# Kernel tuning notes

Hardware: AMD Instinct MI355X
Metric: run time of the kernel (lower is better)

Reference implementation:

```python
import jax, jax.numpy as jnp
import numpy as np

# Static block node counts (src of layer l has N[l] nodes, dst has N[l+1])
N = [100000, 50000, 25000, 12500]
E = [750000, 250000, 125000]
D = 128          # in_feats == n_hidden
E_PAIR = 10000   # pos/neg pair-graph edges
BN_EPS = 1e-5


def setup_inputs() -> dict:
    key = jax.random.key(0)
    ks = jax.random.split(key, 32)
    inp = {}
    inp['x'] = jax.random.normal(ks[0], (N[0], D), dtype=jnp.float32)
    for l in range(3):
        inp[f'src{l}'] = jax.random.randint(ks[1 + 2 * l], (E[l],), 0, N[l], dtype=jnp.int32)
        inp[f'dst{l}'] = jax.random.randint(ks[2 + 2 * l], (E[l],), 0, N[l + 1], dtype=jnp.int32)
    inp['perm'] = jax.random.permutation(ks[7], N[0]).astype(jnp.int32)
    inp['pos_src'] = jax.random.randint(ks[8], (E_PAIR,), 0, N[3], dtype=jnp.int32)
    inp['pos_dst'] = jax.random.randint(ks[9], (E_PAIR,), 0, N[3], dtype=jnp.int32)
    inp['neg_src'] = jax.random.randint(ks[10], (E_PAIR,), 0, N[3], dtype=jnp.int32)
    inp['neg_dst'] = jax.random.randint(ks[11], (E_PAIR,), 0, N[3], dtype=jnp.int32)
    s = 1.0 / np.sqrt(D)
    ki = 12
    for l in range(3):
        inp[f'Wself{l}'] = jax.random.normal(ks[ki], (D, D), dtype=jnp.float32) * s; ki += 1
        inp[f'Wneigh{l}'] = jax.random.normal(ks[ki], (D, D), dtype=jnp.float32) * s; ki += 1
        inp[f'b{l}'] = jnp.zeros((D,), dtype=jnp.float32)
    for l in range(2):
        inp[f'gamma{l}'] = jnp.ones((D,), dtype=jnp.float32)
        inp[f'beta{l}'] = jnp.zeros((D,), dtype=jnp.float32)
    inp['disc_W'] = jax.random.uniform(ks[ki], (D, D), dtype=jnp.float32, minval=-s, maxval=s); ki += 1
    inp['pW1'] = jax.random.normal(ks[ki], (D, D), dtype=jnp.float32) * s; ki += 1
    inp['pb1'] = jnp.zeros((D,), dtype=jnp.float32)
    inp['pW2'] = jax.random.normal(ks[ki], (D, D), dtype=jnp.float32) * s; ki += 1
    inp['pb2'] = jnp.zeros((D,), dtype=jnp.float32)
    inp['pW3'] = jax.random.normal(ks[ki], (D, 1), dtype=jnp.float32) * s; ki += 1
    inp['pb3'] = jnp.zeros((1,), dtype=jnp.float32)
    return inp


def _sage(h, src, dst, n_dst, Wself, Wneigh, b):
    # DGL SAGEConv('mean'): fc_self(h_dst) + fc_neigh(mean over in-neighbors)
    agg = jax.ops.segment_sum(h[src], dst, num_segments=n_dst)          # [n_dst, D]
    deg = jax.ops.segment_sum(jnp.ones(src.shape, h.dtype), dst, num_segments=n_dst)
    mean = agg / jnp.clip(deg, 1.0)[:, None]
    return h[:n_dst] @ Wself + mean @ Wneigh + b


def _bn(h, g, b):
    m = h.mean(0)
    v = h.var(0)
    return g * (h - m) * jax.lax.rsqrt(v + BN_EPS) + b


def _encode(h, blocks, params):
    for l in range(3):
        src, dst, n_dst = blocks[l]
        Ws, Wn, b, g, be = params[l]
        h = _sage(h, src, dst, n_dst, Ws, Wn, b)
        if l != 2:
            h = jax.nn.relu(_bn(h, g, be))  # dropout rate 0
    return h


def reference(x, src0, dst0, src1, dst1, src2, dst2, perm,
              pos_src, pos_dst, neg_src, neg_dst,
              Wself0, Wneigh0, b0, Wself1, Wneigh1, b1, Wself2, Wneigh2, b2,
              gamma0, beta0, gamma1, beta1, disc_W,
              pW1, pb1, pW2, pb2, pW3, pb3):
    blocks = [(src0, dst0, N[1]), (src1, dst1, N[2]), (src2, dst2, N[3])]
    params = [(Wself0, Wneigh0, b0, gamma0, beta0),
              (Wself1, Wneigh1, b1, gamma1, beta1),
              (Wself2, Wneigh2, b2, None, None)]
    positive = _encode(x, blocks, params)          # [N3, D]
    negative = _encode(x[perm], blocks, params)    # corruption: permuted features
    summary = jax.nn.sigmoid(positive.mean(0))     # [D]
    ws = disc_W @ summary                          # [D]
    pos = positive @ ws                            # [N3]
    neg = negative @ ws
    l1 = jnp.mean(jax.nn.softplus(-pos))           # BCEWithLogits vs ones
    l2 = jnp.mean(jax.nn.softplus(neg))            # BCEWithLogits vs zeros

    def predictor(z):
        z = jax.nn.relu(z @ pW1 + pb1)
        z = jax.nn.relu(z @ pW2 + pb2)
        return z @ pW3 + pb3

    h_pos = predictor(positive[pos_src] * positive[pos_dst])  # [E_PAIR, 1]
    h_neg = predictor(positive[neg_src] * positive[neg_dst])
    return h_pos, h_neg, l1 + l2
```

## Files before the change

kernel.cpp:

```cpp
#include <hip/hip_runtime.h>
#include <hip/hip_bf16.h>

#define DD 128
#define BN_EPS 1e-5f
#define NBLK 160
#define ALD 264
#define PLD 136

typedef __hip_bfloat16 bf16;
typedef __attribute__((ext_vector_type(8))) short short8;
typedef __attribute__((ext_vector_type(4))) float f32x4;

__device__ __forceinline__ float b2f(unsigned short u) {
    union { float f; unsigned int i; } x; x.i = ((unsigned int)u) << 16; return x.f;
}
__device__ __forceinline__ unsigned short f2bs(float v) {
    bf16 h = __float2bfloat16(v);
    return *(unsigned short*)&h;
}

__global__ void detect_dtype(const unsigned int* __restrict__ x, int* __restrict__ flag) {
    __shared__ int s[256];
    int t = threadIdx.x;
    unsigned int u = x[t];
    unsigned int e = (u >> 7) & 0xFFu;
    s[t] = ((e >= 90u && e <= 140u) || ((u & 0xFFFFu) == 0u)) ? 1 : 0;
    __syncthreads();
    for (int off = 128; off > 0; off >>= 1) { if (t < off) s[t] += s[t + off]; __syncthreads(); }
    if (t == 0) *flag = (s[0] >= 128) ? 1 : 0;
}

struct CvtTable {
    const void* src[20];
    int off[20];
    int n[20];
    int total;
};
__global__ __launch_bounds__(256) void cvt_all(CvtTable tab, float* __restrict__ wsf,
                                               const int* __restrict__ flagp) {
    int i = blockIdx.x * 256 + threadIdx.x;
    if (i >= tab.total) return;
    int k = 0;
    while (i >= tab.n[k]) { i -= tab.n[k]; ++k; }
    float v;
    if (*flagp) v = b2f(((const unsigned short*)tab.src[k])[i]);
    else        v = ((const float*)tab.src[k])[i];
    wsf[tab.off[k] + i] = v;
}

struct WfAll {
    const float* W1[5];
    const float* W2[5];
    unsigned short* dst[5];
    int KS[5];
    int start[5];
    int total;
};
__global__ __launch_bounds__(256) void wfrag_all(WfAll w) {
    int t = blockIdx.x * 256 + threadIdx.x;
    if (t >= w.total) return;
    int k = 0;
    while (k < 4 && t >= w.start[k + 1]) ++k;
    int lt = t - w.start[k];
    int KS = w.KS[k];
    int lane = lt & 63;
    int ks = (lt >> 6) % KS;
    int ct = lt / (KS * 64);
    int n = ct * 16 + (lane & 15);
    unsigned short v[8];
#pragma unroll
    for (int j = 0; j < 8; ++j) {
        int kk = ks * 32 + ((lane >> 4) & 3) * 8 + j;
        float wv = (kk < 128) ? w.W1[k][kk * DD + n] : w.W2[k][(kk - 128) * DD + n];
        v[j] = f2bs(wv);
    }
    *(uint4*)&w.dst[k][(size_t)lt * 8] = *(uint4*)v;
}

__global__ __launch_bounds__(256) void hist_win(
    const int* __restrict__ d0, int e0, const int* __restrict__ d1, int e1,
    const int* __restrict__ d2, int e2, int* __restrict__ hist) {
    int stride = gridDim.x * 256;
    int t0 = blockIdx.x * 256 + threadIdx.x;
    for (int w = 0; w < 4; ++w) {
        int dlo = w * 12500, dhi = dlo + 12500;
        for (int e = t0; e < e0; e += stride) {
            int d = d0[e];
            if (d >= dlo && d < dhi) atomicAdd(&hist[d], 1);
        }
    }
    for (int e = t0; e < e1; e += stride) atomicAdd(&hist[50000 + d1[e]], 1);
    for (int e = t0; e < e2; e += stride) atomicAdd(&hist[75000 + d2[e]], 1);
}

__global__ __launch_bounds__(256) void scan_bsum(const int* __restrict__ cnt, int n,
                                                 int* __restrict__ bsums) {
    __shared__ int sm[256];
    int t = threadIdx.x, b = blockIdx.x;
    int i4 = b * 256 + t;
    int local = 0;
    if (i4 * 4 < n) { int4 v = ((const int4*)cnt)[i4]; local = v.x + v.y + v.z + v.w; }
    sm[t] = local;
    __syncthreads();
    for (int off = 128; off > 0; off >>= 1) { if (t < off) sm[t] += sm[t + off]; __syncthreads(); }
    if (t == 0) bsums[b] = sm[0];
}
__global__ void scan_bscan(int* __restrict__ bsums, int nb, int* __restrict__ rowptr_n) {
    __shared__ int wsum[4];
    int t = threadIdx.x, lane = t & 63, w = t >> 6;
    int v = (t < nb) ? bsums[t] : 0;
    int inc = v;
    for (int off = 1; off < 64; off <<= 1) {
        int u = __shfl_up(inc, off, 64);
        if (lane >= off) inc += u;
    }
    if (lane == 63) wsum[w] = inc;
    __syncthreads();
    int wo = 0;
    for (int i = 0; i < w; ++i) wo += wsum[i];
    if (t < nb) bsums[t] = wo + inc - v;
    if (t == 255) *rowptr_n = wo + inc;
}
__global__ __launch_bounds__(256) void scan_apply(const int* __restrict__ cnt, int n,
                                                  const int* __restrict__ bsums,
                                                  int* __restrict__ rowptr) {
    __shared__ int wsum[4];
    int t = threadIdx.x, b = blockIdx.x, lane = t & 63, w = t >> 6;
    int i4 = b * 256 + t;
    int4 v = {0, 0, 0, 0};
    bool valid = (i4 * 4 < n);
    if (valid) v = ((const int4*)cnt)[i4];
    int local = v.x + v.y + v.z + v.w;
    int inc = local;
    for (int off = 1; off < 64; off <<= 1) {
        int u = __shfl_up(inc, off, 64);
        if (lane >= off) inc += u;
    }
    if (lane == 63) wsum[w] = inc;
    __syncthreads();
    int wo = 0;
    for (int i = 0; i < w; ++i) wo += wsum[i];
    if (valid) {
        int acc = bsums[b] + wo + inc - local;
        int base = i4 * 4;
        rowptr[base + 0] = acc; acc += v.x;
        rowptr[base + 1] = acc; acc += v.y;
        rowptr[base + 2] = acc; acc += v.z;
        rowptr[base + 3] = acc;
    }
}

__global__ __launch_bounds__(256) void csr_fill_win(
    const int* __restrict__ s0, const int* __restrict__ d0, int e0,
    const int* __restrict__ s1, const int* __restrict__ d1, int e1,
    const int* __restrict__ s2, const int* __restrict__ d2, int e2,
    const int* __restrict__ rpAll, int* __restrict__ cur, int* __restrict__ eid) {
    int stride = gridDim.x * 256;
    int t0 = blockIdx.x * 256 + threadIdx.x;
    for (int w = 0; w < 4; ++w) {
        int dlo = w * 12500, dhi = dlo + 12500;
        for (int e = t0; e < e0; e += stride) {
            int d = d0[e];
            if (d >= dlo && d < dhi)
                eid[rpAll[d] + atomicAdd(&cur[d], 1)] = s0[e];
        }
    }
    for (int e = t0; e < e1; e += stride) {
        int gd = 50000 + d1[e];
        eid[rpAll[gd] + atomicAdd(&cur[gd], 1)] = s1[e];
    }
    for (int e = t0; e < e2; e += stride) {
        int gd = 75000 + d2[e];
        eid[rpAll[gd] + atomicAdd(&cur[gd], 1)] = s2[e];
    }
}

__global__ __launch_bounds__(256) void gather2(
    const void* __restrict__ hvP, const void* __restrict__ hvN,
    const int* __restrict__ flagp,
    const int* __restrict__ permP, const int* __restrict__ permN,
    const float* __restrict__ scP, const float* __restrict__ shP,
    const float* __restrict__ scN, const float* __restrict__ shN,
    const int* __restrict__ rowptr, const int* __restrict__ eid,
    int N, int nRows, unsigned short* __restrict__ out)
{
    int row = blockIdx.x * 4 + (threadIdx.x >> 6);
    int lane = threadIdx.x & 63;
    if (row >= nRows) return;
    int half = row >= N;
    int d = half ? row - N : row;
    const void* hv = half ? hvN : hvP;
    const int* perm = half ? permN : permP;
    const float* sc = half ? scN : scP;
    const float* sh = half ? shN : shP;
    int i0 = rowptr[d], i1 = rowptr[d + 1];
    int abf = flagp ? *flagp : 1;
    bool bn = (sc != nullptr);
    float c0 = 1.0f, c1 = 1.0f, h0 = 0.0f, h1 = 0.0f;
    if (bn) { c0 = sc[lane * 2]; c1 = sc[lane * 2 + 1]; h0 = sh[lane * 2]; h1 = sh[lane * 2 + 1]; }

#define XF0(v) (bn ? fmaxf(c0 * (v) + h0, 0.0f) : (v))
#define XF1(v) (bn ? fmaxf(c1 * (v) + h1, 0.0f) : (v))
    float ax[8] = {}, ay[8] = {};
    int i = i0;
    if (abf) {
        const unsigned short* h = (const unsigned short*)hv;
        for (; i + 8 <= i1; i += 8) {
            int sI[8];
#pragma unroll
            for (int j = 0; j < 8; ++j) sI[j] = eid[i + j];
            if (perm) {
#pragma unroll
                for (int j = 0; j < 8; ++j) sI[j] = perm[sI[j]];
            }
            ushort2 v[8];
#pragma unroll
            for (int j = 0; j < 8; ++j) v[j] = *(const ushort2*)&h[(size_t)sI[j] * DD + lane * 2];
#pragma unroll
            for (int j = 0; j < 8; ++j) { ax[j] += XF0(b2f(v[j].x)); ay[j] += XF1(b2f(v[j].y)); }
        }
        for (; i < i1; ++i) {
            int s = eid[i];
            if (perm) s = perm[s];
            ushort2 v = *(const ushort2*)&h[(size_t)s * DD + lane * 2];
            ax[0] += XF0(b2f(v.x)); ay[0] += XF1(b2f(v.y));
        }
    } else {
        const float* h = (const float*)hv;
        for (; i + 8 <= i1; i += 8) {
            int sI[8];
#pragma unroll
            for (int j = 0; j < 8; ++j) sI[j] = eid[i + j];
            if (perm) {
#pragma unroll
                for (int j = 0; j < 8; ++j) sI[j] = perm[sI[j]];
            }
            float2 v[8];
#pragma unroll
            for (int j = 0; j < 8; ++j) v[j] = *(const float2*)&h[(size_t)sI[j] * DD + lane * 2];
#pragma unroll
            for (int j = 0; j < 8; ++j) { ax[j] += XF0(v[j].x); ay[j] += XF1(v[j].y); }
        }
        for (; i < i1; ++i) {
            int s = eid[i];
            if (perm) s = perm[s];
            float2 v = *(const float2*)&h[(size_t)s * DD + lane * 2];
            ax[0] += XF0(v.x); ay[0] += XF1(v.y);
        }
    }
#undef XF0
#undef XF1
    float sx = (ax[0] + ax[1]) + (ax[2] + ax[3]) + (ax[4] + ax[5]) + (ax[6] + ax[7]);
    float sy = (ay[0] + ay[1]) + (ay[2] + ay[3]) + (ay[4] + ay[5]) + (ay[6] + ay[7]);
    float rd = 1.0f / fmaxf((float)(i1 - i0), 1.0f);
    ushort2 o;
    o.x = f2bs(sx * rd);
    o.y = f2bs(sy * rd);
    *(ushort2*)&out[(size_t)row * DD + lane * 2] = o;
}

struct GHalf {
    const void* A1;
    const int* gather;
    const float* sc;
    const float* sh;
    const unsigned short* A2;
    unsigned short* out;
    float* PS;
    float* PQ;
};
__global__ __launch_bounds__(256) void mfma_gemm2(
    GHalf hP, GHalf hN, const int* __restrict__ flagp,
    const uint4* __restrict__ wfrag, const float* __restrict__ bias,
    int Nh, int nbHalf)
{
    __shared__ unsigned short As[64 * ALD];
    __shared__ float sds[256];
    const int tid = threadIdx.x;
    const int half = blockIdx.x / nbHalf;
    const int rb = (blockIdx.x % nbHalf) * 64;
    const GHalf H = half ? hN : hP;
    const int abf = flagp ? *flagp : 1;
    const bool bn = (H.sc != nullptr);
    const bool doStats = (H.PS != nullptr);

    {
        int r = tid >> 2, cs = (tid & 3) * 32;
        int gr = rb + r;
        unsigned short* dst = &As[r * ALD + cs];
        if (gr < Nh) {
            int ar = H.gather ? H.gather[gr] : gr;
            if (abf) {
                const unsigned short* s = (const unsigned short*)H.A1 + (size_t)ar * DD + cs;
                if (bn) {
#pragma unroll
                    for (int i = 0; i < 32; ++i) {
                        float v = b2f(s[i]);
                        v = fmaxf(H.sc[cs + i] * v + H.sh[cs + i], 0.0f);
                        dst[i] = f2bs(v);
                    }
                } else {
                    const uint4* sv = (const uint4*)s;
                    uint4* dv = (uint4*)dst;
#pragma unroll
                    for (int i = 0; i < 4; ++i) dv[i] = sv[i];
                }
            } else {
                const float* s = (const float*)H.A1 + (size_t)ar * DD + cs;
#pragma unroll
                for (int i = 0; i < 32; ++i) dst[i] = f2bs(s[i]);
            }
            const uint4* s2 = (const uint4*)(H.A2 + (size_t)gr * DD + cs);
            uint4* d2 = (uint4*)(dst + 128);
#pragma unroll
            for (int i = 0; i < 4; ++i) d2[i] = s2[i];
        } else {
            uint4 z = {0, 0, 0, 0};
            uint4* dv = (uint4*)dst;
#pragma unroll
            for (int i = 0; i < 4; ++i) dv[i] = z;
            uint4* d2 = (uint4*)(dst + 128);
#pragma unroll
            for (int i = 0; i < 4; ++i) d2[i] = z;
        }
    }
    if (doStats) { sds[tid] = 0.0f; }
    __syncthreads();

    const int w = tid >> 6, lane = tid & 63;
    const int m0 = w * 16;
    f32x4 acc[8] = {};
    for (int ks = 0; ks < 8; ++ks) {
        short8 a = *(const short8*)&As[(m0 + (lane & 15)) * ALD + ks * 32 + ((lane >> 4) & 3) * 8];
#pragma unroll
        for (int ct = 0; ct < 8; ++ct) {
            uint4 braw = wfrag[(ct * 8 + ks) * 64 + lane];
            short8 b = *(short8*)&braw;
            acc[ct] = __builtin_amdgcn_mfma_f32_16x16x32_bf16(a, b, acc[ct], 0, 0, 0);
        }
    }

#pragma unroll
    for (int ct = 0; ct < 8; ++ct) {
        int col = ct * 16 + (lane & 15);
        float bv = bias[col];
        float sv = 0.0f, sq = 0.0f;
#pragma unroll
        for (int r = 0; r < 4; ++r) {
            int grow = rb + m0 + ((lane >> 4) & 3) * 4 + r;
            float v = acc[ct][r] + bv;
            if (grow < Nh) {
                H.out[(size_t)grow * DD + col] = f2bs(v);
                sv += v; sq += v * v;
            }
        }
        if (doStats) {
            sv += __shfl_down(sv, 32, 64); sv += __shfl_down(sv, 16, 64);
            sq += __shfl_down(sq, 32, 64); sq += __shfl_down(sq, 16, 64);
            if (lane < 16) {
                atomicAdd(&sds[ct * 16 + lane], sv);
                atomicAdd(&sds[128 + ct * 16 + lane], sq);
            }
        }
    }
    if (doStats) {
        __syncthreads();
        if (tid < 128) {
            H.PS[(blockIdx.x % nbHalf) * 128 + tid] = sds[tid];
            H.PQ[(blockIdx.x % nbHalf) * 128 + tid] = sds[128 + tid];
        }
    }
}

__global__ __launch_bounds__(256) void pred_gemm(
    const unsigned short* __restrict__ A,
    const unsigned short* __restrict__ PF,
    const int* __restrict__ ps, const int* __restrict__ pd,
    const int* __restrict__ ns, const int* __restrict__ nd, int EPc,
    const uint4* __restrict__ wfrag, const float* __restrict__ bias,
    unsigned short* __restrict__ out, int Mc)
{
    __shared__ unsigned short As[64 * PLD];
    const int tid = threadIdx.x;
    const int rb = blockIdx.x * 64;

    {
        int r = tid >> 2, cs = (tid & 3) * 32;
        int gr = rb + r;
        unsigned short* dst = &As[r * PLD + cs];
        if (gr < Mc) {
            if (ps) {
                int a = (gr < EPc) ? ps[gr] : ns[gr - EPc];
                int b = (gr < EPc) ? pd[gr] : nd[gr - EPc];
                const unsigned short* ra = PF + (size_t)a * DD + cs;
                const unsigned short* rbp = PF + (size_t)b * DD + cs;
#pragma unroll
                for (int i = 0; i < 32; ++i)
                    dst[i] = f2bs(b2f(ra[i]) * b2f(rbp[i]));
            } else {
                const uint4* sv = (const uint4*)(A + (size_t)gr * DD + cs);
                uint4* dv = (uint4*)dst;
#pragma unroll
                for (int i = 0; i < 4; ++i) dv[i] = sv[i];
            }
        } else {
            uint4 z = {0, 0, 0, 0};
            uint4* dv = (uint4*)dst;
#pragma unroll
            for (int i = 0; i < 4; ++i) dv[i] = z;
        }
    }
    __syncthreads();

    const int w = tid >> 6, lane = tid & 63;
    const int m0 = w * 16;
    f32x4 acc[8] = {};
    for (int ks = 0; ks < 4; ++ks) {
        short8 a = *(const short8*)&As[(m0 + (lane & 15)) * PLD + ks * 32 + ((lane >> 4) & 3) * 8];
#pragma unroll
        for (int ct = 0; ct < 8; ++ct) {
            uint4 braw = wfrag[(ct * 4 + ks) * 64 + lane];
            short8 b = *(short8*)&braw;
            acc[ct] = __builtin_amdgcn_mfma_f32_16x16x32_bf16(a, b, acc[ct], 0, 0, 0);
        }
    }

#pragma unroll
    for (int ct = 0; ct < 8; ++ct) {
        int col = ct * 16 + (lane & 15);
        float bv = bias[col];
#pragma unroll
        for (int r = 0; r < 4; ++r) {
            int grow = rb + m0 + ((lane >> 4) & 3) * 4 + r;
            if (grow >= Mc) continue;
            float v = fmaxf(acc[ct][r] + bv, 0.0f);
            out[(size_t)grow * DD + col] = f2bs(v);
        }
    }
}

__global__ __launch_bounds__(256) void p2bn_fast(
    const float* __restrict__ PSa, const float* __restrict__ PQa,
    float* __restrict__ sca, float* __restrict__ sha,
    const float* __restrict__ PSb, const float* __restrict__ PQb,
    float* __restrict__ scb, float* __restrict__ shb,
    int nb, int M,
    const float* __restrict__ gamma, const float* __restrict__ beta)
{
    int tensor = blockIdx.x >> 7, col = blockIdx.x & 127;
    const float* PS = tensor ? PSb : PSa;
    const float* PQ = tensor ? PQb : PQa;
    float* sc = tensor ? scb : sca;
    float* sh = tensor ? shb : sha;
    __shared__ float sS[256], sQ[256];
    int t = threadIdx.x;
    float s = 0.0f, q = 0.0f;
    for (int b = t; b < nb; b += 256) {
        s += PS[b * 128 + col];
        q += PQ[b * 128 + col];
    }
    sS[t] = s; sQ[t] = q;
    __syncthreads();
    for (int off = 128; off > 0; off >>= 1) {
        if (t < off) { sS[t] += sS[t + off]; sQ[t] += sQ[t + off]; }
        __syncthreads();
    }
    if (t == 0) {
        float m = sS[0] / (float)M;
        float var = fmaxf(sQ[0] / (float)M - m * m, 0.0f);
        float inv = rsqrtf(var + BN_EPS);
        float g = gamma[col];
        sc[col] = g * inv;
        sh[col] = beta[col] - g * m * inv;
    }
}

__global__ __launch_bounds__(256) void colreduce(const float* __restrict__ PS, int nb,
                                                 float* __restrict__ out) {
    __shared__ float sS[256];
    int col = blockIdx.x;
    int t = threadIdx.x;
    float s = 0.0f;
    for (int b = t; b < nb; b += 256) s += PS[b * 128 + col];
    sS[t] = s;
    __syncthreads();
    for (int off = 128; off > 0; off >>= 1) { if (t < off) sS[t] += sS[t + off]; __syncthreads(); }
    if (t == 0) out[col] = sS[0];
}

__global__ void make_ws(const float* __restrict__ colsum, const float* __restrict__ discW,
                        float* __restrict__ wsv, int M) {
    __shared__ float s[128];
    int t = threadIdx.x;
    s[t] = 1.0f / (1.0f + expf(-(colsum[t] / (float)M)));
    __syncthreads();
    float acc = 0.0f;
#pragma unroll
    for (int j = 0; j < 128; ++j) acc += discW[t * 128 + j] * s[j];
    wsv[t] = acc;
}

__global__ __launch_bounds__(256) void loss_partial(
    const unsigned short* __restrict__ P, const unsigned short* __restrict__ Ng,
    const float* __restrict__ wsv, float* __restrict__ lossP, float* __restrict__ lossN, int M)
{
    __shared__ float sP[4], sN[4];
    int lane = threadIdx.x & 63;
    int wave = threadIdx.x >> 6;
    int gw = blockIdx.x * 4 + wave;
    int nw = gridDim.x * 4;
    float w0 = wsv[lane], w1 = wsv[lane + 64];
    float accP = 0.0f, accN = 0.0f;
    for (int row = gw; row < 2 * M; row += nw) {
        const unsigned short* base = (row < M) ? &P[(size_t)row * DD]
                                               : &Ng[(size_t)(row - M) * DD];
        float a = b2f(base[lane]) * w0 + b2f(base[lane + 64]) * w1;
#pragma unroll
        for (int off = 32; off > 0; off >>= 1) a += __shfl_down(a, off, 64);
        if (lane == 0) {
            float x = (row < M) ? -a : a;
            float sp = fmaxf(x, 0.0f) + log1pf(expf(-fabsf(x)));
            if (row < M) accP += sp; else accN += sp;
        }
    }
    if (lane == 0) { sP[wave] = accP; sN[wave] = accN; }
    __syncthreads();
    if (threadIdx.x == 0) {
        lossP[blockIdx.x] = sP[0] + sP[1] + sP[2] + sP[3];
        lossN[blockIdx.x] = sN[0] + sN[1] + sN[2] + sN[3];
    }
}

__global__ void write_loss(const float* __restrict__ lossP, const float* __restrict__ lossN,
                           void* __restrict__ outv, int M, const int* __restrict__ flagp) {
    __shared__ float s[256];
    int t = threadIdx.x;
    s[t] = (t < NBLK) ? (lossP[t] + lossN[t]) : 0.0f;
    __syncthreads();
    for (int off = 128; off > 0; off >>= 1) { if (t < off) s[t] += s[t + off]; __syncthreads(); }
    if (t == 0) {
        float v = s[0] / (float)M;
        if (*flagp) ((bf16*)outv)[20000] = __float2bfloat16(v);
        else        ((float*)outv)[20000] = v;
    }
}

__global__ __launch_bounds__(256) void final_mv(
    const unsigned short* __restrict__ ZB, const float* __restrict__ pW3,
    const float* __restrict__ pb3,
    void* __restrict__ outv, int nRows, const int* __restrict__ flagp) {
    int row = blockIdx.x * 4 + (threadIdx.x >> 6);
    int lane = threadIdx.x & 63;
    if (row >= nRows) return;
    float a = b2f(ZB[(size_t)row * DD + lane]) * pW3[lane]
            + b2f(ZB[(size_t)row * DD + lane + 64]) * pW3[lane + 64];
#pragma unroll
    for (int off = 32; off > 0; off >>= 1) a += __shfl_down(a, off, 64);
    if (lane == 0) {
        float v = a + pb3[0];
        if (*flagp) ((bf16*)outv)[row] = __float2bfloat16(v);
        else        ((float*)outv)[row] = v;
    }
}

extern "C" void kernel_launch(void* const* d_in, const int* in_sizes, int n_in,
                              void* d_out, int out_size, void* d_ws, size_t ws_size,
                              hipStream_t stream)
{
    const void* x      = d_in[0];
    const int* srcA[3] = {(const int*)d_in[1], (const int*)d_in[3], (const int*)d_in[5]};
    const int* dstA[3] = {(const int*)d_in[2], (const int*)d_in[4], (const int*)d_in[6]};
    const int* perm    = (const int*)d_in[7];
    const int* pos_src = (const int*)d_in[8];
    const int* pos_dst = (const int*)d_in[9];
    const int* neg_src = (const int*)d_in[10];
    const int* neg_dst = (const int*)d_in[11];

    const int N1 = 50000, N2 = 25000, N3 = 12500;
    const int E[3] = {750000, 250000, 125000};
    const int EP = 10000;
    const int NCAT = 87500;

    float* wsf = (float*)d_ws;
    int*   wsi = (int*)d_ws;
    int*   flagp = wsi;
    float* lossP = wsf + 64;
    float* lossN = wsf + 224;
    float* wsvec = wsf + 512;
    float* scP0 = wsf + 640;  float* shP0 = wsf + 768;
    float* scN0 = wsf + 896;  float* shN0 = wsf + 1024;
    float* scP1 = wsf + 1152; float* shP1 = wsf + 1280;
    float* scN1 = wsf + 1408; float* shN1 = wsf + 1536;
    int*   bsums = wsi + 1664;
    float* colsum = wsf + 1920;
    float* PSP = wsf + 2048;
    float* PQP = wsf + 102400;
    float* PSN = wsf + 202752;
    float* PQN = wsf + 303104;
    int* histAll = wsi + 403456;
    int* curAll  = wsi + 491008;
    int* rpAll   = wsi + 578560;
    int* eidAll  = wsi + 666112;
    const size_t WfB = 1791232;
    float* WS[3] = {wsf + WfB, wsf + WfB + 32896, wsf + WfB + 65792};
    float* WN[3] = {wsf + WfB + 16384, wsf + WfB + 49280, wsf + WfB + 82176};
    float* BV[3] = {wsf + WfB + 32768, wsf + WfB + 65664, wsf + WfB + 98560};
    float* G0  = wsf + WfB + 98688;  float* BE0 = wsf + WfB + 98816;
    float* G1  = wsf + WfB + 98944;  float* BE1 = wsf + WfB + 99072;
    float* DW  = wsf + WfB + 99200;
    float* PW1 = wsf + WfB + 115584; float* PB1 = wsf + WfB + 131968;
    float* PW2 = wsf + WfB + 132096; float* PB2 = wsf + WfB + 148480;
    float* PW3 = wsf + WfB + 148608; float* PB3 = wsf + WfB + 148736;
    unsigned short* wfragL[3] = {(unsigned short*)(wsf + 1940480),
                                 (unsigned short*)(wsf + 1956864),
                                 (unsigned short*)(wsf + 1973248)};
    unsigned short* wfragP[2] = {(unsigned short*)(wsf + 1989632),
                                 (unsigned short*)(wsf + 1997824)};
    unsigned short* PF  = (unsigned short*)(wsf + 2006016);
    unsigned short* NF  = (unsigned short*)(wsf + 2806016);
    unsigned short* H2P = (unsigned short*)(wsf + 3606016);
    unsigned short* H2N = (unsigned short*)(wsf + 5206016);
    unsigned short* H1P = (unsigned short*)(wsf + 6806016);
    unsigned short* H1N = (unsigned short*)(wsf + 10006016);
    unsigned short* AGG = (unsigned short*)(wsf + 13206016);
    unsigned short* ZA = H1N;
    unsigned short* ZB = H1N + (size_t)2560000;

    detect_dtype<<<1, 256, 0, stream>>>((const unsigned int*)x, flagp);
    CvtTable tab;
    const int widx[20] = {12,13,14, 15,16,17, 18,19,20, 21,22,23,24, 25, 26,27, 28,29, 30,31};
    float* wdst[20] = {WS[0],WN[0],BV[0], WS[1],WN[1],BV[1], WS[2],WN[2],BV[2],
                       G0,BE0,G1,BE1, DW, PW1,PB1, PW2,PB2, PW3,PB3};
    const int wn[20] = {16384,16384,128, 16384,16384,128, 16384,16384,128,
                        128,128,128,128, 16384, 16384,128, 16384,128, 128,1};
    int tot = 0;
    for (int k = 0; k < 20; ++k) {
        tab.src[k] = d_in[widx[k]];
        tab.off[k] = (int)(wdst[k] - wsf);
        tab.n[k] = wn[k];
        tot += wn[k];
    }
    tab.total = tot;
    cvt_all<<<(tot + 255) / 256, 256, 0, stream>>>(tab, wsf, flagp);

    hipMemsetAsync(histAll, 0, (size_t)(2 * NCAT + 128) * 4, stream);
    hist_win<<<512, 256, 0, stream>>>(dstA[0], E[0], dstA[1], E[1], dstA[2], E[2], histAll);
    {
        int nb = (NCAT / 4 + 255) / 256;
        scan_bsum<<<nb, 256, 0, stream>>>(histAll, NCAT, bsums);
        scan_bscan<<<1, 256, 0, stream>>>(bsums, nb, rpAll + NCAT);
        scan_apply<<<nb, 256, 0, stream>>>(histAll, NCAT, bsums, rpAll);
    }
    csr_fill_win<<<512, 256, 0, stream>>>(
        srcA[0], dstA[0], E[0], srcA[1], dstA[1], E[1], srcA[2], dstA[2], E[2],
        rpAll, curAll, eidAll);

    WfAll wa;
    wa.W1[0] = WS[0]; wa.W2[0] = WN[0]; wa.dst[0] = wfragL[0]; wa.KS[0] = 8; wa.start[0] = 0;
    wa.W1[1] = WS[1]; wa.W2[1] = WN[1]; wa.dst[1] = wfragL[1]; wa.KS[1] = 8; wa.start[1] = 4096;
    wa.W1[2] = WS[2]; wa.W2[2] = WN[2]; wa.dst[2] = wfragL[2]; wa.KS[2] = 8; wa.start[2] = 8192;
    wa.W1[3] = PW1;   wa.W2[3] = nullptr; wa.dst[3] = wfragP[0]; wa.KS[3] = 4; wa.start[3] = 12288;
    wa.W1[4] = PW2;   wa.W2[4] = nullptr; wa.dst[4] = wfragP[1]; wa.KS[4] = 4; wa.start[4] = 14336;
    wa.total = 16384;
    wfrag_all<<<64, 256, 0, stream>>>(wa);

    const int nb0 = (N1 + 63) / 64, nb1 = (N2 + 63) / 64, nb2 = (N3 + 63) / 64;

    gather2<<<(N1 + 3) / 4, 256, 0, stream>>>(
        x, x, flagp, nullptr, nullptr, nullptr, nullptr, nullptr, nullptr,
        rpAll, eidAll, N1, N1, AGG);
    {
        GHalf hP = {x, nullptr, nullptr, nullptr, AGG, H1P, PSP, PQP};
        mfma_gemm2<<<nb0, 256, 0, stream>>>(hP, hP, flagp, (const uint4*)wfragL[0], BV[0], N1, nb0);
    }
    gather2<<<(N1 + 3) / 4, 256, 0, stream>>>(
        x, x, flagp, perm, perm, nullptr, nullptr, nullptr, nullptr,
        rpAll, eidAll, N1, N1, AGG);
    {
        GHalf hN = {x, perm, nullptr, nullptr, AGG, H1N, PSN, PQN};
        mfma_gemm2<<<nb0, 256, 0, stream>>>(hN, hN, flagp, (const uint4*)wfragL[0], BV[0], N1, nb0);
    }
    p2bn_fast<<<256, 256, 0, stream>>>(PSP, PQP, scP0, shP0, PSN, PQN, scN0, shN0, nb0, N1, G0, BE0);

    gather2<<<(2 * N2 + 3) / 4, 256, 0, stream>>>(
        H1P, H1N, nullptr, nullptr, nullptr, scP0, shP0, scN0, shN0,
        rpAll + 50000, eidAll, N2, 2 * N2, AGG);
    {
        GHalf hP = {H1P, nullptr, scP0, shP0, AGG,                      H2P, PSP, PQP};
        GHalf hN = {H1N, nullptr, scN0, shN0, AGG + (size_t)N2 * DD,    H2N, PSN, PQN};
        mfma_gemm2<<<2 * nb1, 256, 0, stream>>>(hP, hN, nullptr, (const uint4*)wfragL[1], BV[1], N2, nb1);
    }
    p2bn_fast<<<256, 256, 0, stream>>>(PSP, PQP, scP1, shP1, PSN, PQN, scN1, shN1, nb1, N2, G1, BE1);

    gather2<<<(2 * N3 + 3) / 4, 256, 0, stream>>>(
        H2P, H2N, nullptr, nullptr, nullptr, scP1, shP1, scN1, shN1,
        rpAll + 75000, eidAll, N3, 2 * N3, AGG);
    {
        GHalf hP = {H2P, nullptr, scP1, shP1, AGG,                      PF, PSP, PQP};
        GHalf hN = {H2N, nullptr, scN1, shN1, AGG + (size_t)N3 * DD,    NF, nullptr, nullptr};
        mfma_gemm2<<<2 * nb2, 256, 0, stream>>>(hP, hN, nullptr, (const uint4*)wfragL[2], BV[2], N3, nb2);
    }
    colreduce<<<128, 256, 0, stream>>>(PSP, nb2, colsum);
    make_ws<<<1, 128, 0, stream>>>(colsum, DW, wsvec, N3);

    loss_partial<<<NBLK, 256, 0, stream>>>(PF, NF, wsvec, lossP, lossN, N3);
    write_loss<<<1, 256, 0, stream>>>(lossP, lossN, d_out, N3, flagp);

    pred_gemm<<<(2 * EP + 63) / 64, 256, 0, stream>>>(
        nullptr, PF, pos_src, pos_dst, neg_src, neg_dst, EP,
        (const uint4*)wfragP[0], PB1, ZA, 2 * EP);
    pred_gemm<<<(2 * EP + 63) / 64, 256, 0, stream>>>(
        ZA, nullptr, nullptr, nullptr, nullptr, nullptr, 0,
        (const uint4*)wfragP[1], PB2, ZB, 2 * EP);
    final_mv<<<(2 * EP + 3) / 4, 256, 0, stream>>>(ZB, PW3, PB3, d_out, 2 * EP, flagp);
}
```

Measured before the change: 664.6 us.

## Batch layer-0 pos/neg gather and GEMM, flatten histogram, shrink gather unroll

When the workspace is large enough, the layer-0 positive and negative gathers and GEMMs are merged into one gather launch and one GEMM launch over twice the rows, using a second AGG region. This removes launches and serialization and gives each launch more blocks. The histogram kernel drops its four-pass windowed loop over layer-0 edges and becomes a single pass with one thread per edge. The gather inner loop goes from 8-way to 4-way unroll, which cuts register use at the cost of fewer loads in flight.

```diff
diff --git a/kernel.cpp b/kernel.cpp
--- a/kernel.cpp
+++ b/kernel.cpp
@@ -77,20 +77,13 @@
     *(uint4*)&w.dst[k][(size_t)lt * 8] = *(uint4*)v;
 }
 
-__global__ __launch_bounds__(256) void hist_win(
+__global__ __launch_bounds__(256) void hist_all(
     const int* __restrict__ d0, int e0, const int* __restrict__ d1, int e1,
     const int* __restrict__ d2, int e2, int* __restrict__ hist) {
-    int stride = gridDim.x * 256;
-    int t0 = blockIdx.x * 256 + threadIdx.x;
-    for (int w = 0; w < 4; ++w) {
-        int dlo = w * 12500, dhi = dlo + 12500;
-        for (int e = t0; e < e0; e += stride) {
-            int d = d0[e];
-            if (d >= dlo && d < dhi) atomicAdd(&hist[d], 1);
-        }
-    }
-    for (int e = t0; e < e1; e += stride) atomicAdd(&hist[50000 + d1[e]], 1);
-    for (int e = t0; e < e2; e += stride) atomicAdd(&hist[75000 + d2[e]], 1);
+    int e = blockIdx.x * 256 + threadIdx.x;
+    if (e < e0) atomicAdd(&hist[d0[e]], 1);
+    else if (e < e0 + e1) atomicAdd(&hist[50000 + d1[e - e0]], 1);
+    else if (e < e0 + e1 + e2) atomicAdd(&hist[75000 + d2[e - e0 - e1]], 1);
 }
 
 __global__ __launch_bounds__(256) void scan_bsum(const int* __restrict__ cnt, int n,
@@ -201,61 +194,55 @@
 
 #define XF0(v) (bn ? fmaxf(c0 * (v) + h0, 0.0f) : (v))
 #define XF1(v) (bn ? fmaxf(c1 * (v) + h1, 0.0f) : (v))
-    float ax[8] = {}, ay[8] = {};
+    float a0x = 0, a0y = 0, a1x = 0, a1y = 0, a2x = 0, a2y = 0, a3x = 0, a3y = 0;
     int i = i0;
     if (abf) {
         const unsigned short* h = (const unsigned short*)hv;
-        for (; i + 8 <= i1; i += 8) {
-            int sI[8];
-#pragma unroll
-            for (int j = 0; j < 8; ++j) sI[j] = eid[i + j];
-            if (perm) {
-#pragma unroll
-                for (int j = 0; j < 8; ++j) sI[j] = perm[sI[j]];
-            }
-            ushort2 v[8];
-#pragma unroll
-            for (int j = 0; j < 8; ++j) v[j] = *(const ushort2*)&h[(size_t)sI[j] * DD + lane * 2];
-#pragma unroll
-            for (int j = 0; j < 8; ++j) { ax[j] += XF0(b2f(v[j].x)); ay[j] += XF1(b2f(v[j].y)); }
+        for (; i + 4 <= i1; i += 4) {
+            int s0 = eid[i], s1 = eid[i + 1], s2 = eid[i + 2], s3 = eid[i + 3];
+            if (perm) { s0 = perm[s0]; s1 = perm[s1]; s2 = perm[s2]; s3 = perm[s3]; }
+            ushort2 v0 = *(const ushort2*)&h[(size_t)s0 * DD + lane * 2];
+            ushort2 v1 = *(const ushort2*)&h[(size_t)s1 * DD + lane * 2];
+            ushort2 v2 = *(const ushort2*)&h[(size_t)s2 * DD + lane * 2];
+            ushort2 v3 = *(const ushort2*)&h[(size_t)s3 * DD + lane * 2];
+            a0x += XF0(b2f(v0.x)); a0y += XF1(b2f(v0.y));
+            a1x += XF0(b2f(v1.x)); a1y += XF1(b2f(v1.y));
+            a2x += XF0(b2f(v2.x)); a2y += XF1(b2f(v2.y));
+            a3x += XF0(b2f(v3.x)); a3y += XF1(b2f(v3.y));
         }
         for (; i < i1; ++i) {
             int s = eid[i];
             if (perm) s = perm[s];
             ushort2 v = *(const ushort2*)&h[(size_t)s * DD + lane * 2];
-            ax[0] += XF0(b2f(v.x)); ay[0] += XF1(b2f(v.y));
+            a0x += XF0(b2f(v.x)); a0y += XF1(b2f(v.y));
         }
     } else {
         const float* h = (const float*)hv;
-        for (; i + 8 <= i1; i += 8) {
-            int sI[8];
-#pragma unroll
-            for (int j = 0; j < 8; ++j) sI[j] = eid[i + j];
-            if (perm) {
-#pragma unroll
-                for (int j = 0; j < 8; ++j) sI[j] = perm[sI[j]];
-            }
-            float2 v[8];
-#pragma unroll
-            for (int j = 0; j < 8; ++j) v[j] = *(const float2*)&h[(size_t)sI[j] * DD + lane * 2];
-#pragma unroll
-            for (int j = 0; j < 8; ++j) { ax[j] += XF0(v[j].x); ay[j] += XF1(v[j].y); }
+        for (; i + 4 <= i1; i += 4) {
+            int s0 = eid[i], s1 = eid[i + 1], s2 = eid[i + 2], s3 = eid[i + 3];
+            if (perm) { s0 = perm[s0]; s1 = perm[s1]; s2 = perm[s2]; s3 = perm[s3]; }
+            float2 v0 = *(const float2*)&h[(size_t)s0 * DD + lane * 2];
+            float2 v1 = *(const float2*)&h[(size_t)s1 * DD + lane * 2];
+            float2 v2 = *(const float2*)&h[(size_t)s2 * DD + lane * 2];
+            float2 v3 = *(const float2*)&h[(size_t)s3 * DD + lane * 2];
+            a0x += XF0(v0.x); a0y += XF1(v0.y);
+            a1x += XF0(v1.x); a1y += XF1(v1.y);
+            a2x += XF0(v2.x); a2y += XF1(v2.y);
+            a3x += XF0(v3.x); a3y += XF1(v3.y);
         }
         for (; i < i1; ++i) {
             int s = eid[i];
             if (perm) s = perm[s];
             float2 v = *(const float2*)&h[(size_t)s * DD + lane * 2];
-            ax[0] += XF0(v.x); ay[0] += XF1(v.y);
+            a0x += XF0(v.x); a0y += XF1(v.y);
         }
     }
 #undef XF0
 #undef XF1
-    float sx = (ax[0] + ax[1]) + (ax[2] + ax[3]) + (ax[4] + ax[5]) + (ax[6] + ax[7]);
-    float sy = (ay[0] + ay[1]) + (ay[2] + ay[3]) + (ay[4] + ay[5]) + (ay[6] + ay[7]);
     float rd = 1.0f / fmaxf((float)(i1 - i0), 1.0f);
     ushort2 o;
-    o.x = f2bs(sx * rd);
-    o.y = f2bs(sy * rd);
+    o.x = f2bs((a0x + a1x + a2x + a3x) * rd);
+    o.y = f2bs((a0y + a1y + a2y + a3y) * rd);
     *(ushort2*)&out[(size_t)row * DD + lane * 2] = o;
 }
 
@@ -626,6 +613,8 @@
     unsigned short* ZA = H1N;
     unsigned short* ZB = H1N + (size_t)2560000;
 
+    const bool bigWS = ws_size >= (size_t)(13206016 + 6400000) * 4;
+
     detect_dtype<<<1, 256, 0, stream>>>((const unsigned int*)x, flagp);
     CvtTable tab;
     const int widx[20] = {12,13,14, 15,16,17, 18,19,20, 21,22,23,24, 25, 26,27, 28,29, 30,31};
@@ -644,7 +633,9 @@
     cvt_all<<<(tot + 255) / 256, 256, 0, stream>>>(tab, wsf, flagp);
 
     hipMemsetAsync(histAll, 0, (size_t)(2 * NCAT + 128) * 4, stream);
-    hist_win<<<512, 256, 0, stream>>>(dstA[0], E[0], dstA[1], E[1], dstA[2], E[2], histAll);
+    int Etot = E[0] + E[1] + E[2];
+    hist_all<<<(Etot + 255) / 256, 256, 0, stream>>>(
+        dstA[0], E[0], dstA[1], E[1], dstA[2], E[2], histAll);
     {
         int nb = (NCAT / 4 + 255) / 256;
         scan_bsum<<<nb, 256, 0, stream>>>(histAll, NCAT, bsums);
@@ -666,19 +657,28 @@
 
     const int nb0 = (N1 + 63) / 64, nb1 = (N2 + 63) / 64, nb2 = (N3 + 63) / 64;
 
-    gather2<<<(N1 + 3) / 4, 256, 0, stream>>>(
-        x, x, flagp, nullptr, nullptr, nullptr, nullptr, nullptr, nullptr,
-        rpAll, eidAll, N1, N1, AGG);
-    {
-        GHalf hP = {x, nullptr, nullptr, nullptr, AGG, H1P, PSP, PQP};
-        mfma_gemm2<<<nb0, 256, 0, stream>>>(hP, hP, flagp, (const uint4*)wfragL[0], BV[0], N1, nb0);
-    }
-    gather2<<<(N1 + 3) / 4, 256, 0, stream>>>(
-        x, x, flagp, perm, perm, nullptr, nullptr, nullptr, nullptr,
-        rpAll, eidAll, N1, N1, AGG);
-    {
-        GHalf hN = {x, perm, nullptr, nullptr, AGG, H1N, PSN, PQN};
-        mfma_gemm2<<<nb0, 256, 0, stream>>>(hN, hN, flagp, (const uint4*)wfragL[0], BV[0], N1, nb0);
+    if (bigWS) {
+        gather2<<<(2 * N1 + 3) / 4, 256, 0, stream>>>(
+            x, x, flagp, nullptr, perm, nullptr, nullptr, nullptr, nullptr,
+            rpAll, eidAll, N1, 2 * N1, AGG);
+        GHalf hP = {x, nullptr, nullptr, nullptr, AGG,                       H1P, PSP, PQP};
+        GHalf hN = {x, perm,    nullptr, nullptr, AGG + (size_t)N1 * DD,     H1N, PSN, PQN};
+        mfma_gemm2<<<2 * nb0, 256, 0, stream>>>(hP, hN, flagp, (const uint4*)wfragL[0], BV[0], N1, nb0);
+    } else {
+        gather2<<<(N1 + 3) / 4, 256, 0, stream>>>(
+            x, x, flagp, nullptr, nullptr, nullptr, nullptr, nullptr, nullptr,
+            rpAll, eidAll, N1, N1, AGG);
+        {
+            GHalf hP = {x, nullptr, nullptr, nullptr, AGG, H1P, PSP, PQP};
+            mfma_gemm2<<<nb0, 256, 0, stream>>>(hP, hP, flagp, (const uint4*)wfragL[0], BV[0], N1, nb0);
+        }
+        gather2<<<(N1 + 3) / 4, 256, 0, stream>>>(
+            x, x, flagp, perm, perm, nullptr, nullptr, nullptr, nullptr,
+            rpAll, eidAll, N1, N1, AGG);
+        {
+            GHalf hN = {x, perm, nullptr, nullptr, AGG, H1N, PSN, PQN};
+            mfma_gemm2<<<nb0, 256, 0, stream>>>(hN, hN, flagp, (const uint4*)wfragL[0], BV[0], N1, nb0);
+        }
     }
     p2bn_fast<<<256, 256, 0, stream>>>(PSP, PQP, scP0, shP0, PSN, PQN, scN0, shN0, nb0, N1, G0, BE0);
 
```

After: 628.6 us. 5.4% less time.
